# Kernel optimization log

Hardware: AMD Instinct MI355X
Metric: run time of the kernel (lower is better)

The kernel has to match this reference:

```python
import jax, jax.numpy as jnp
import numpy as np
from jax import lax

# Model constants (from init_kwargs + canonical Mamba defaults)
VOCAB = 32000
D_MODEL = 512
N_LAYERS = 6
D_INNER = 2 * D_MODEL          # expand=2
D_STATE = 16
D_CONV = 4
DT_RANK = D_MODEL // 16        # 32
B, L = 2, 1024
EPS = 1e-5


def setup_inputs() -> dict:
    key = jax.random.key(0)
    ks = jax.random.split(key, 12)
    s = 0.02
    # A initialized as in mamba_ssm: A = 1..d_state repeated over channels
    A = jnp.tile(jnp.arange(1, D_STATE + 1, dtype=jnp.float32), (D_INNER, 1))  # [d_inner, d_state]
    A_log = jnp.tile(jnp.log(A)[None], (N_LAYERS, 1, 1))
    return {
        "tokens": jax.random.randint(ks[0], (B, L), 0, VOCAB),
        "embed": jax.random.normal(ks[1], (VOCAB, D_MODEL), jnp.float32) * s,
        "in_proj_w": jax.random.normal(ks[2], (N_LAYERS, 2 * D_INNER, D_MODEL), jnp.float32) * s,
        "conv_w": jax.random.normal(ks[3], (N_LAYERS, D_INNER, 1, D_CONV), jnp.float32) * 0.2,
        "conv_b": jnp.zeros((N_LAYERS, D_INNER), jnp.float32),
        "x_proj_w": jax.random.normal(ks[4], (N_LAYERS, DT_RANK + 2 * D_STATE, D_INNER), jnp.float32) * s,
        "dt_proj_w": jax.random.normal(ks[5], (N_LAYERS, D_INNER, DT_RANK), jnp.float32) * 0.1,
        "dt_proj_b": jnp.full((N_LAYERS, D_INNER), -4.0, jnp.float32),  # softplus -> small dt
        "A_log": A_log,
        "D_skip": jnp.ones((N_LAYERS, D_INNER), jnp.float32),
        "out_proj_w": jax.random.normal(ks[6], (N_LAYERS, D_MODEL, D_INNER), jnp.float32) * s,
        "norm_w": jnp.ones((D_MODEL,), jnp.float32),
        "norm_b": jnp.zeros((D_MODEL,), jnp.float32),
        "head_w": jax.random.normal(ks[7], (VOCAB, D_MODEL), jnp.float32) * s,
    }


def _selective_scan(dA, dBu, C):
    # dA, dBu: [b, l, d, n]; C: [b, l, n] -> y: [b, l, d]
    def step(h, inp):
        dA_t, dBu_t, c_t = inp          # [b,d,n], [b,d,n], [b,n]
        h = dA_t * h + dBu_t
        return h, jnp.einsum("bdn,bn->bd", h, c_t)
    h0 = jnp.zeros(dA.shape[:1] + dA.shape[2:], dA.dtype)  # [b, d, n]
    _, ys = lax.scan(step, h0, (jnp.moveaxis(dA, 1, 0), jnp.moveaxis(dBu, 1, 0), jnp.moveaxis(C, 1, 0)))
    return jnp.moveaxis(ys, 0, 1)


def _mamba_block(x, inw, cw, cb, xpw, dtw, dtb, A_log, Dp, outw):
    # x: [b, l, d_model]
    xz = jnp.einsum("bld,ed->ble", x, inw)            # [b, l, 2*d_inner]
    xi, z = jnp.split(xz, 2, axis=-1)                  # each [b, l, d_inner]
    # causal depthwise conv1d
    xc = jnp.moveaxis(xi, 1, 2)                        # [b, d_inner, l]
    xc = lax.conv_general_dilated(xc, cw, (1,), [(D_CONV - 1, 0)],
                                  feature_group_count=D_INNER)
    xi = jax.nn.silu(jnp.moveaxis(xc + cb[None, :, None], 1, 2))  # [b, l, d_inner]
    # input-dependent dt, B, C
    dbc = jnp.einsum("bld,ed->ble", xi, xpw)           # [b, l, dt_rank+2*d_state]
    dt, Bm, Cm = jnp.split(dbc, [DT_RANK, DT_RANK + D_STATE], axis=-1)
    delta = jax.nn.softplus(jnp.einsum("blr,dr->bld", dt, dtw) + dtb)  # [b, l, d_inner]
    A = -jnp.exp(A_log)                                # [d_inner, d_state]
    dA = jnp.exp(delta[..., None] * A)                 # [b, l, d_inner, d_state]
    dBu = (delta * xi)[..., None] * Bm[:, :, None, :]  # [b, l, d_inner, d_state]
    y = _selective_scan(dA, dBu, Cm) + xi * Dp         # [b, l, d_inner]
    y = y * jax.nn.silu(z)
    return jnp.einsum("ble,de->bld", y, outw)          # [b, l, d_model]


def reference(tokens, embed, in_proj_w, conv_w, conv_b, x_proj_w, dt_proj_w,
              dt_proj_b, A_log, D_skip, out_proj_w, norm_w, norm_b, head_w):
    x = embed[tokens]                                  # [b, l, d_model]
    for i in range(N_LAYERS):
        x = _mamba_block(x, in_proj_w[i], conv_w[i], conv_b[i], x_proj_w[i],
                         dt_proj_w[i], dt_proj_b[i], A_log[i], D_skip[i], out_proj_w[i])
    mu = jnp.mean(x, axis=-1, keepdims=True)
    var = jnp.mean(jnp.square(x - mu), axis=-1, keepdims=True)
    x = (x - mu) * lax.rsqrt(var + EPS) * norm_w + norm_b
    logits = jnp.einsum("bld,vd->blv", x, head_w)      # [b, l, vocab]
    return logits
```

## Files before the change

### kernel.cpp

```cpp
#include <hip/hip_runtime.h>
#include <hip/hip_bf16.h>
#include <cstdint>
#include <cstddef>

#define VOCAB 32000
#define DMODEL 512
#define NLAYERS 6
#define DINNER 1024
#define DSTATE 16
#define DCONV 4
#define DTRANK 32
#define BB 2
#define LL 1024
#define ROWS (BB * LL)

typedef _Float16 half8 __attribute__((ext_vector_type(8)));
typedef float floatx4 __attribute__((ext_vector_type(4)));

__global__ __launch_bounds__(128) void embed_k(const int* __restrict__ tokens,
                                               const float* __restrict__ embed,
                                               float* __restrict__ x) {
    int row = blockIdx.x;
    int tid = threadIdx.x;
    int tok = tokens[row];
    *(float4*)(x + (size_t)row * DMODEL + tid * 4) =
        *(const float4*)(embed + (size_t)tok * DMODEL + tid * 4);
}

template<int BM, int BN>
__global__ __launch_bounds__(256) void gemm_split(
    const float* __restrict__ A, int lda,
    const float* __restrict__ W, int ldw,
    float* __restrict__ C, int ldc,
    int K, int NBX)
{
    constexpr int FM = BM / 32;
    constexpr int FN = BN / 32;
    __shared__ __attribute__((aligned(16))) _Float16 As[BM * 64];
    __shared__ __attribute__((aligned(16))) _Float16 Bs[BN * 64];

    int bid = blockIdx.x;
    int cpx = gridDim.x >> 3;
    int swz = (bid & 7) * cpx + (bid >> 3);
    int bx = swz % NBX, by = swz / NBX;
    int m0 = by * BM, n0 = bx * BN;

    int tid = threadIdx.x;
    int wid = tid >> 6, lane = tid & 63;
    int wm = wid >> 1, wn = wid & 1;
    int lr = lane & 15, lk = lane >> 4;

    floatx4 acc[FM][FN] = {};

    constexpr int ACH = BM * 4;
    constexpr int TOT = (BM + BN) * 4;

    for (int k0 = 0; k0 < K; k0 += 32) {
#pragma unroll
        for (int i = tid; i < TOT; i += 256) {
            bool isA = i < ACH;
            int j = isA ? i : i - ACH;
            int r = j >> 2, c8 = j & 3;
            const float* src = isA ? (A + (size_t)(m0 + r) * lda + k0 + c8 * 8)
                                   : (W + (size_t)(n0 + r) * ldw + k0 + c8 * 8);
            float4 v0 = *(const float4*)(src);
            float4 v1 = *(const float4*)(src + 4);
            float vv[8] = {v0.x, v0.y, v0.z, v0.w, v1.x, v1.y, v1.z, v1.w};
            half8 hi, lo;
#pragma unroll
            for (int e = 0; e < 8; ++e) {
                _Float16 h = (_Float16)vv[e];
                hi[e] = h;
                lo[e] = (_Float16)(vv[e] - (float)h);
            }
            _Float16* dst = (isA ? As : Bs) + r * 64;
            *(half8*)(dst + (((c8)     ^ (r & 7)) << 3)) = hi;
            *(half8*)(dst + (((c8 + 4) ^ (r & 7)) << 3)) = lo;
        }
        __syncthreads();

        half8 ah[FM], al[FM], bh[FN], bl[FN];
#pragma unroll
        for (int f = 0; f < FM; ++f) {
            int r = wm * (BM / 2) + f * 16 + lr;
            const _Float16* p = As + r * 64;
            ah[f] = *(const half8*)(p + (((lk)     ^ (r & 7)) << 3));
            al[f] = *(const half8*)(p + (((lk + 4) ^ (r & 7)) << 3));
        }
#pragma unroll
        for (int f = 0; f < FN; ++f) {
            int r = wn * (BN / 2) + f * 16 + lr;
            const _Float16* p = Bs + r * 64;
            bh[f] = *(const half8*)(p + (((lk)     ^ (r & 7)) << 3));
            bl[f] = *(const half8*)(p + (((lk + 4) ^ (r & 7)) << 3));
        }
#pragma unroll
        for (int i2 = 0; i2 < FM; ++i2)
#pragma unroll
            for (int j2 = 0; j2 < FN; ++j2) {
                acc[i2][j2] = __builtin_amdgcn_mfma_f32_16x16x32_f16(ah[i2], bh[j2], acc[i2][j2], 0, 0, 0);
                acc[i2][j2] = __builtin_amdgcn_mfma_f32_16x16x32_f16(ah[i2], bl[j2], acc[i2][j2], 0, 0, 0);
                acc[i2][j2] = __builtin_amdgcn_mfma_f32_16x16x32_f16(al[i2], bh[j2], acc[i2][j2], 0, 0, 0);
            }
        __syncthreads();
    }

#pragma unroll
    for (int f = 0; f < FM; ++f)
#pragma unroll
        for (int g = 0; g < FN; ++g) {
            int row = m0 + wm * (BM / 2) + f * 16 + (lane >> 4) * 4;
            int col = n0 + wn * (BN / 2) + g * 16 + (lane & 15);
#pragma unroll
            for (int j = 0; j < 4; ++j)
                C[(size_t)(row + j) * ldc + col] = acc[f][g][j];
        }
}

__global__ __launch_bounds__(256) void gemm_nt(
    const float* __restrict__ A, int lda,
    const float* __restrict__ W, int ldw,
    float* __restrict__ C, int ldc,
    int M, int N, int K,
    const float* __restrict__ bias, int epi)
{
    __shared__ float As[16][64];
    __shared__ float Bs[16][64];
    int tid = threadIdx.x;
    int tx = tid & 15, ty = tid >> 4;
    int m0 = blockIdx.y * 64, n0 = blockIdx.x * 64;
    int lr = tid >> 2;
    int lc = (tid & 3) * 4;
    float acc[4][4] = {};

    for (int k0 = 0; k0 < K; k0 += 16) {
        float4 a4 = *(const float4*)(A + (size_t)(m0 + lr) * lda + k0 + lc);
        float4 b4 = *(const float4*)(W + (size_t)(n0 + lr) * ldw + k0 + lc);
        As[lc + 0][lr] = a4.x; As[lc + 1][lr] = a4.y;
        As[lc + 2][lr] = a4.z; As[lc + 3][lr] = a4.w;
        Bs[lc + 0][lr] = b4.x; Bs[lc + 1][lr] = b4.y;
        Bs[lc + 2][lr] = b4.z; Bs[lc + 3][lr] = b4.w;
        __syncthreads();
#pragma unroll
        for (int k = 0; k < 16; ++k) {
            float4 av = *(const float4*)&As[k][ty * 4];
            float4 bv = *(const float4*)&Bs[k][tx * 4];
            float a_[4] = {av.x, av.y, av.z, av.w};
            float b_[4] = {bv.x, bv.y, bv.z, bv.w};
#pragma unroll
            for (int i = 0; i < 4; ++i)
#pragma unroll
                for (int j = 0; j < 4; ++j)
                    acc[i][j] += a_[i] * b_[j];
        }
        __syncthreads();
    }

#pragma unroll
    for (int i = 0; i < 4; ++i) {
        int row = m0 + ty * 4 + i;
        int col = n0 + tx * 4;
        float v[4] = {acc[i][0], acc[i][1], acc[i][2], acc[i][3]};
        if (epi == 1) {
#pragma unroll
            for (int j = 0; j < 4; ++j) {
                float t = v[j] + bias[col + j];
                v[j] = (t > 20.f) ? t : log1pf(expf(t));
            }
        }
        float4 o = {v[0], v[1], v[2], v[3]};
        *(float4*)(C + (size_t)row * ldc + col) = o;
    }
}

__global__ __launch_bounds__(256) void conv_silu(const float* __restrict__ xz,
                                                 const float* __restrict__ cw,
                                                 const float* __restrict__ cb,
                                                 float* __restrict__ xi) {
    int idx = blockIdx.x * 256 + threadIdx.x;
    int d = idx & 1023;
    int t = (idx >> 10) & 1023;
    int b = idx >> 20;
    const float* base = xz + (size_t)(b * LL) * (2 * DINNER) + d;
    float acc = cb[d];
#pragma unroll
    for (int j = 0; j < DCONV; ++j) {
        int tt = t - 3 + j;
        if (tt >= 0) acc += cw[d * 4 + j] * base[(size_t)tt * (2 * DINNER)];
    }
    float s = acc / (1.f + expf(-acc));
    xi[idx] = s;
}

template <int PASS>
__global__ __launch_bounds__(256) void scan_k(
    const float* __restrict__ dlt, const float* __restrict__ xi,
    const float* __restrict__ dbc, const float* __restrict__ A_log,
    const float* __restrict__ Dskip, const float* __restrict__ xz,
    float* __restrict__ P, float* __restrict__ S,
    const float* __restrict__ H0, float* __restrict__ yg)
{
    __shared__ float sd[128][16], sx[128][16], sB[128][16], sC[128][16], sY[128][16];
    int c = blockIdx.x, dblk = blockIdx.y, b = blockIdx.z;
    int tid = threadIdx.x;
    int d0 = dblk * 16;
    int t0 = c * 128;

    for (int idx = tid; idx < 128 * 16; idx += 256) {
        int t = idx >> 4, i = idx & 15;
        int row = b * LL + t0 + t;
        sd[t][i] = dlt[(size_t)row * DINNER + d0 + i];
        sx[t][i] = xi[(size_t)row * DINNER + d0 + i];
        sB[t][i] = dbc[(size_t)row * 64 + DTRANK + i];
        sC[t][i] = dbc[(size_t)row * 64 + DTRANK + DSTATE + i];
    }
    __syncthreads();

    int di = tid >> 4, n = tid & 15;
    int d = d0 + di;
    float Adn = -expf(A_log[d * DSTATE + n]);
    float Dsk = Dskip[d];
    float h, ap = 1.f;
    if (PASS == 1) h = 0.f;
    else           h = H0[(size_t)(c * 2 + b) * 16384 + d * 16 + n];

    for (int t = 0; t < 128; ++t) {
        float dl = sd[t][di];
        float dA = expf(dl * Adn);
        h = dA * h + dl * sx[t][di] * sB[t][n];
        if (PASS == 1) {
            ap *= dA;
        } else {
            float p = h * sC[t][n];
            p += __shfl_xor(p, 1);
            p += __shfl_xor(p, 2);
            p += __shfl_xor(p, 4);
            p += __shfl_xor(p, 8);
            if (n == 0) sY[t][di] = p + sx[t][di] * Dsk;
        }
    }

    if (PASS == 1) {
        size_t o = (size_t)(c * 2 + b) * 16384 + d * 16 + n;
        P[o] = ap;
        S[o] = h;
    } else {
        __syncthreads();
        for (int idx = tid; idx < 128 * 16; idx += 256) {
            int t = idx >> 4, i = idx & 15;
            int row = b * LL + t0 + t;
            float z = xz[(size_t)row * (2 * DINNER) + DINNER + d0 + i];
            float y = sY[t][i];
            yg[(size_t)row * DINNER + d0 + i] = y * (z / (1.f + expf(-z)));
        }
    }
}

__global__ __launch_bounds__(256) void scan_carry(const float* __restrict__ P,
                                                  const float* __restrict__ S,
                                                  float* __restrict__ H0) {
    int idx = blockIdx.x * 256 + threadIdx.x;
    float carry = 0.f;
#pragma unroll
    for (int c = 0; c < 8; ++c) {
        H0[(size_t)c * 32768 + idx] = carry;
        carry = P[(size_t)c * 32768 + idx] * carry + S[(size_t)c * 32768 + idx];
    }
}

__global__ __launch_bounds__(128) void lnorm(const float* __restrict__ x,
                                             const float* __restrict__ w,
                                             const float* __restrict__ bp,
                                             float* __restrict__ xn) {
    int row = blockIdx.x;
    int tid = threadIdx.x;
    float4 v = *(const float4*)(x + (size_t)row * DMODEL + tid * 4);
    float s = v.x + v.y + v.z + v.w;
    float q = v.x * v.x + v.y * v.y + v.z * v.z + v.w * v.w;
#pragma unroll
    for (int m = 1; m < 64; m <<= 1) {
        s += __shfl_xor(s, m);
        q += __shfl_xor(q, m);
    }
    __shared__ float ss[2], qq[2];
    if ((tid & 63) == 0) { ss[tid >> 6] = s; qq[tid >> 6] = q; }
    __syncthreads();
    s = ss[0] + ss[1];
    q = qq[0] + qq[1];
    float mu = s / (float)DMODEL;
    float var = q / (float)DMODEL - mu * mu;
    float r = rsqrtf(var + 1e-5f);
    int c = tid * 4;
    float4 o;
    o.x = (v.x - mu) * r * w[c + 0] + bp[c + 0];
    o.y = (v.y - mu) * r * w[c + 1] + bp[c + 1];
    o.z = (v.z - mu) * r * w[c + 2] + bp[c + 2];
    o.w = (v.w - mu) * r * w[c + 3] + bp[c + 3];
    *(float4*)(xn + (size_t)row * DMODEL + c) = o;
}

extern "C" void kernel_launch(void* const* d_in, const int* in_sizes, int n_in,
                              void* d_out, int out_size, void* d_ws, size_t ws_size,
                              hipStream_t stream) {
    const int*   tokens = (const int*)d_in[0];
    const float* embed  = (const float*)d_in[1];
    const float* inw    = (const float*)d_in[2];
    const float* cw     = (const float*)d_in[3];
    const float* cb     = (const float*)d_in[4];
    const float* xpw    = (const float*)d_in[5];
    const float* dtw    = (const float*)d_in[6];
    const float* dtb    = (const float*)d_in[7];
    const float* Alog   = (const float*)d_in[8];
    const float* Dsk    = (const float*)d_in[9];
    const float* outw   = (const float*)d_in[10];
    const float* nw     = (const float*)d_in[11];
    const float* nb     = (const float*)d_in[12];
    const float* hw     = (const float*)d_in[13];
    float* out = (float*)d_out;

    float* ws = (float*)d_ws;
    float* x   = ws;
    float* xz  = x   + (1 << 20);
    float* xib = xz  + (4 << 20);
    float* dbc = xib + (2 << 20);
    float* dlt = dbc + (1 << 17);
    float* yg  = dlt + (2 << 20);
    float* xn  = yg  + (2 << 20);
    float* Pb  = xn  + (1 << 20);
    float* Sb  = Pb  + (1 << 18);
    float* H0  = Sb  + (1 << 18);

    embed_k<<<ROWS, 128, 0, stream>>>(tokens, embed, x);

    for (int l = 0; l < NLAYERS; ++l) {
        const float* inw_l  = inw  + (size_t)l * 2 * DINNER * DMODEL;
        const float* cw_l   = cw   + (size_t)l * DINNER * DCONV;
        const float* cb_l   = cb   + (size_t)l * DINNER;
        const float* xpw_l  = xpw  + (size_t)l * 64 * DINNER;
        const float* dtw_l  = dtw  + (size_t)l * DINNER * DTRANK;
        const float* dtb_l  = dtb  + (size_t)l * DINNER;
        const float* Alog_l = Alog + (size_t)l * DINNER * DSTATE;
        const float* Dsk_l  = Dsk  + (size_t)l * DINNER;
        const float* outw_l = outw + (size_t)l * DMODEL * DINNER;

        gemm_split<128, 128><<<16 * 16, 256, 0, stream>>>(
            x, DMODEL, inw_l, DMODEL, xz, 2 * DINNER, DMODEL, 16);
        conv_silu<<<(ROWS * DINNER) / 256, 256, 0, stream>>>(xz, cw_l, cb_l, xib);
        gemm_nt<<<dim3(1, ROWS / 64), 256, 0, stream>>>(
            xib, DINNER, xpw_l, DINNER, dbc, 64, ROWS, 64, DINNER, nullptr, 0);
        gemm_nt<<<dim3(DINNER / 64, ROWS / 64), 256, 0, stream>>>(
            dbc, 64, dtw_l, DTRANK, dlt, DINNER, ROWS, DINNER, DTRANK, dtb_l, 1);
        scan_k<1><<<dim3(8, DINNER / 16, BB), 256, 0, stream>>>(
            dlt, xib, dbc, Alog_l, Dsk_l, xz, Pb, Sb, nullptr, nullptr);
        scan_carry<<<128, 256, 0, stream>>>(Pb, Sb, H0);
        scan_k<3><<<dim3(8, DINNER / 16, BB), 256, 0, stream>>>(
            dlt, xib, dbc, Alog_l, Dsk_l, xz, nullptr, nullptr, H0, yg);
        gemm_split<64, 64><<<32 * 8, 256, 0, stream>>>(
            yg, DINNER, outw_l, DINNER, x, DMODEL, DINNER, 8);
    }

    lnorm<<<ROWS, 128, 0, stream>>>(x, nw, nb, xn);
    gemm_split<128, 128><<<250 * 16, 256, 0, stream>>>(
        xn, DMODEL, hw, DMODEL, out, VOCAB, DMODEL, 250);
}
```

Measured before the change: 1.964 ms.

## Fuse dt projection into scan, use MFMA for x_proj, remap head GEMM tiles

```diff
diff --git a/kernel.cpp b/kernel.cpp
--- a/kernel.cpp
+++ b/kernel.cpp
@@ -27,7 +27,7 @@
         *(const float4*)(embed + (size_t)tok * DMODEL + tid * 4);
 }
 
-template<int BM, int BN>
+template<int BM, int BN, int MODE>
 __global__ __launch_bounds__(256) void gemm_split(
     const float* __restrict__ A, int lda,
     const float* __restrict__ W, int ldw,
@@ -40,9 +40,18 @@
     __shared__ __attribute__((aligned(16))) _Float16 Bs[BN * 64];
 
     int bid = blockIdx.x;
-    int cpx = gridDim.x >> 3;
-    int swz = (bid & 7) * cpx + (bid >> 3);
-    int bx = swz % NBX, by = swz / NBX;
+    int bx, by;
+    if (MODE == 1) {
+        int xcd = bid & 7, j = bid >> 3;
+        bx = xcd * 32 + (j >> 4);
+        by = j & 15;
+        if (bx >= NBX) return;
+    } else {
+        int cpx = gridDim.x >> 3;
+        int swz = (bid & 7) * cpx + (bid >> 3);
+        bx = swz % NBX;
+        by = swz / NBX;
+    }
     int m0 = by * BM, n0 = bx * BN;
 
     int tid = threadIdx.x;
@@ -117,62 +126,6 @@
         }
 }
 
-__global__ __launch_bounds__(256) void gemm_nt(
-    const float* __restrict__ A, int lda,
-    const float* __restrict__ W, int ldw,
-    float* __restrict__ C, int ldc,
-    int M, int N, int K,
-    const float* __restrict__ bias, int epi)
-{
-    __shared__ float As[16][64];
-    __shared__ float Bs[16][64];
-    int tid = threadIdx.x;
-    int tx = tid & 15, ty = tid >> 4;
-    int m0 = blockIdx.y * 64, n0 = blockIdx.x * 64;
-    int lr = tid >> 2;
-    int lc = (tid & 3) * 4;
-    float acc[4][4] = {};
-
-    for (int k0 = 0; k0 < K; k0 += 16) {
-        float4 a4 = *(const float4*)(A + (size_t)(m0 + lr) * lda + k0 + lc);
-        float4 b4 = *(const float4*)(W + (size_t)(n0 + lr) * ldw + k0 + lc);
-        As[lc + 0][lr] = a4.x; As[lc + 1][lr] = a4.y;
-        As[lc + 2][lr] = a4.z; As[lc + 3][lr] = a4.w;
-        Bs[lc + 0][lr] = b4.x; Bs[lc + 1][lr] = b4.y;
-        Bs[lc + 2][lr] = b4.z; Bs[lc + 3][lr] = b4.w;
-        __syncthreads();
-#pragma unroll
-        for (int k = 0; k < 16; ++k) {
-            float4 av = *(const float4*)&As[k][ty * 4];
-            float4 bv = *(const float4*)&Bs[k][tx * 4];
-            float a_[4] = {av.x, av.y, av.z, av.w};
-            float b_[4] = {bv.x, bv.y, bv.z, bv.w};
-#pragma unroll
-            for (int i = 0; i < 4; ++i)
-#pragma unroll
-                for (int j = 0; j < 4; ++j)
-                    acc[i][j] += a_[i] * b_[j];
-        }
-        __syncthreads();
-    }
-
-#pragma unroll
-    for (int i = 0; i < 4; ++i) {
-        int row = m0 + ty * 4 + i;
-        int col = n0 + tx * 4;
-        float v[4] = {acc[i][0], acc[i][1], acc[i][2], acc[i][3]};
-        if (epi == 1) {
-#pragma unroll
-            for (int j = 0; j < 4; ++j) {
-                float t = v[j] + bias[col + j];
-                v[j] = (t > 20.f) ? t : log1pf(expf(t));
-            }
-        }
-        float4 o = {v[0], v[1], v[2], v[3]};
-        *(float4*)(C + (size_t)row * ldc + col) = o;
-    }
-}
-
 __global__ __launch_bounds__(256) void conv_silu(const float* __restrict__ xz,
                                                  const float* __restrict__ cw,
                                                  const float* __restrict__ cb,
@@ -194,25 +147,46 @@
 
 template <int PASS>
 __global__ __launch_bounds__(256) void scan_k(
-    const float* __restrict__ dlt, const float* __restrict__ xi,
-    const float* __restrict__ dbc, const float* __restrict__ A_log,
-    const float* __restrict__ Dskip, const float* __restrict__ xz,
+    const float* __restrict__ xi, const float* __restrict__ dbc,
+    const float* __restrict__ dtw, const float* __restrict__ dtb,
+    const float* __restrict__ A_log, const float* __restrict__ Dskip,
+    const float* __restrict__ xz,
     float* __restrict__ P, float* __restrict__ S,
     const float* __restrict__ H0, float* __restrict__ yg)
 {
     __shared__ float sd[128][16], sx[128][16], sB[128][16], sC[128][16], sY[128][16];
+    __shared__ float sdt[16][33];
+    __shared__ float sdb[128][32];
+    __shared__ float sdtb[16];
     int c = blockIdx.x, dblk = blockIdx.y, b = blockIdx.z;
     int tid = threadIdx.x;
     int d0 = dblk * 16;
     int t0 = c * 128;
 
+    for (int idx = tid; idx < 512; idx += 256)
+        sdt[idx >> 5][idx & 31] = dtw[(size_t)(d0 + (idx >> 5)) * DTRANK + (idx & 31)];
+    if (tid < 16) sdtb[tid] = dtb[d0 + tid];
+
     for (int idx = tid; idx < 128 * 16; idx += 256) {
         int t = idx >> 4, i = idx & 15;
-        int row = b * LL + t0 + t;
-        sd[t][i] = dlt[(size_t)row * DINNER + d0 + i];
-        sx[t][i] = xi[(size_t)row * DINNER + d0 + i];
-        sB[t][i] = dbc[(size_t)row * 64 + DTRANK + i];
-        sC[t][i] = dbc[(size_t)row * 64 + DTRANK + DSTATE + i];
+        size_t row = (size_t)(b * LL + t0 + t);
+        sx[t][i] = xi[row * DINNER + d0 + i];
+        sB[t][i] = dbc[row * 64 + DTRANK + i];
+        if (PASS == 3) sC[t][i] = dbc[row * 64 + DTRANK + DSTATE + i];
+    }
+    for (int idx = tid; idx < 128 * 8; idx += 256) {
+        int t = idx >> 3, q = idx & 7;
+        size_t row = (size_t)(b * LL + t0 + t);
+        *(float4*)&sdb[t][q * 4] = *(const float4*)(dbc + row * 64 + q * 4);
+    }
+    __syncthreads();
+
+    for (int idx = tid; idx < 128 * 16; idx += 256) {
+        int t = idx >> 4, i = idx & 15;
+        float a = sdtb[i];
+#pragma unroll
+        for (int k = 0; k < DTRANK; ++k) a += sdb[t][k] * sdt[i][k];
+        sd[t][i] = (a > 20.f) ? a : log1pf(expf(a));
     }
     __syncthreads();
 
@@ -248,10 +222,10 @@
         __syncthreads();
         for (int idx = tid; idx < 128 * 16; idx += 256) {
             int t = idx >> 4, i = idx & 15;
-            int row = b * LL + t0 + t;
-            float z = xz[(size_t)row * (2 * DINNER) + DINNER + d0 + i];
+            size_t row = (size_t)(b * LL + t0 + t);
+            float z = xz[row * (2 * DINNER) + DINNER + d0 + i];
             float y = sY[t][i];
-            yg[(size_t)row * DINNER + d0 + i] = y * (z / (1.f + expf(-z)));
+            yg[row * DINNER + d0 + i] = y * (z / (1.f + expf(-z)));
         }
     }
 }
@@ -323,8 +297,7 @@
     float* xz  = x   + (1 << 20);
     float* xib = xz  + (4 << 20);
     float* dbc = xib + (2 << 20);
-    float* dlt = dbc + (1 << 17);
-    float* yg  = dlt + (2 << 20);
+    float* yg  = dbc + (1 << 17);
     float* xn  = yg  + (2 << 20);
     float* Pb  = xn  + (1 << 20);
     float* Sb  = Pb  + (1 << 18);
@@ -343,23 +316,21 @@
         const float* Dsk_l  = Dsk  + (size_t)l * DINNER;
         const float* outw_l = outw + (size_t)l * DMODEL * DINNER;
 
-        gemm_split<128, 128><<<16 * 16, 256, 0, stream>>>(
+        gemm_split<128, 128, 0><<<16 * 16, 256, 0, stream>>>(
             x, DMODEL, inw_l, DMODEL, xz, 2 * DINNER, DMODEL, 16);
         conv_silu<<<(ROWS * DINNER) / 256, 256, 0, stream>>>(xz, cw_l, cb_l, xib);
-        gemm_nt<<<dim3(1, ROWS / 64), 256, 0, stream>>>(
-            xib, DINNER, xpw_l, DINNER, dbc, 64, ROWS, 64, DINNER, nullptr, 0);
-        gemm_nt<<<dim3(DINNER / 64, ROWS / 64), 256, 0, stream>>>(
-            dbc, 64, dtw_l, DTRANK, dlt, DINNER, ROWS, DINNER, DTRANK, dtb_l, 1);
+        gemm_split<128, 64, 0><<<16, 256, 0, stream>>>(
+            xib, DINNER, xpw_l, DINNER, dbc, 64, DINNER, 1);
         scan_k<1><<<dim3(8, DINNER / 16, BB), 256, 0, stream>>>(
-            dlt, xib, dbc, Alog_l, Dsk_l, xz, Pb, Sb, nullptr, nullptr);
+            xib, dbc, dtw_l, dtb_l, Alog_l, Dsk_l, xz, Pb, Sb, nullptr, nullptr);
         scan_carry<<<128, 256, 0, stream>>>(Pb, Sb, H0);
         scan_k<3><<<dim3(8, DINNER / 16, BB), 256, 0, stream>>>(
-            dlt, xib, dbc, Alog_l, Dsk_l, xz, nullptr, nullptr, H0, yg);
-        gemm_split<64, 64><<<32 * 8, 256, 0, stream>>>(
+            xib, dbc, dtw_l, dtb_l, Alog_l, Dsk_l, xz, nullptr, nullptr, H0, yg);
+        gemm_split<64, 64, 0><<<32 * 8, 256, 0, stream>>>(
             yg, DINNER, outw_l, DINNER, x, DMODEL, DINNER, 8);
     }
 
     lnorm<<<ROWS, 128, 0, stream>>>(x, nw, nb, xn);
-    gemm_split<128, 128><<<250 * 16, 256, 0, stream>>>(
+    gemm_split<128, 128, 1><<<256 * 16, 256, 0, stream>>>(
         xn, DMODEL, hw, DMODEL, out, VOCAB, DMODEL, 250);
 }
```

Result: slower. 2.207 ms (+12.4%).
